# Kernel tuning notes

Hardware: AMD Instinct MI355X
Metric: run time of the kernel (lower is better)

## Reference

```python
import jax, jax.numpy as jnp
import numpy as np

NEG_SLOPE = 0.2  # PyG GATv2Conv default negative_slope


def gatv2_layer(x, src, dst, n_nodes, Wl, bl, Wr, br, att, b_out):
    """GATv2Conv, heads=1, add_self_loops=False.
    x: [N, Din]; src/dst: [E] int; Wl/Wr: [Din, H]; att: [H]."""
    xl = x @ Wl + bl                      # [N, H] source transform
    xr = x @ Wr + br                      # [N, H] target transform
    e = jax.nn.leaky_relu(xl[src] + xr[dst], NEG_SLOPE)  # [E, H]
    logits = e @ att                      # [E]
    # numerically-stable softmax over variable-degree neighborhoods (per dst)
    m = jax.ops.segment_max(logits, dst, num_segments=n_nodes)  # [N]
    m = jnp.where(jnp.isfinite(m), m, 0.0)  # nodes with no in-edges
    p = jnp.exp(logits - m[dst])          # [E]
    denom = jax.ops.segment_sum(p, dst, num_segments=n_nodes)   # [N]
    alpha = p / jnp.maximum(denom[dst], 1e-16)                  # [E]
    out = jax.ops.segment_sum(alpha[:, None] * xl[src], dst, num_segments=n_nodes)
    return out + b_out                    # [N, H]


def setup_inputs() -> dict:
    N, E, D, H = 40000, 640000, 128, 128
    key = jax.random.key(0)
    ks = jax.random.split(key, 12)
    s = 1.0 / np.sqrt(D)
    return {
        "x": jax.random.normal(ks[0], (N, D), dtype=jnp.float32),
        "edge_index": jax.random.randint(ks[1], (2, E), 0, N, dtype=jnp.int64),
        "Wl1": jax.random.normal(ks[2], (D, H), dtype=jnp.float32) * s,
        "bl1": jnp.zeros((H,), jnp.float32),
        "Wr1": jax.random.normal(ks[3], (D, H), dtype=jnp.float32) * s,
        "br1": jnp.zeros((H,), jnp.float32),
        "att1": jax.random.normal(ks[4], (H,), dtype=jnp.float32) * s,
        "b1": jnp.zeros((H,), jnp.float32),
        "Wl2": jax.random.normal(ks[5], (H, H), dtype=jnp.float32) * s,
        "bl2": jnp.zeros((H,), jnp.float32),
        "Wr2": jax.random.normal(ks[6], (H, H), dtype=jnp.float32) * s,
        "br2": jnp.zeros((H,), jnp.float32),
        "att2": jax.random.normal(ks[7], (H,), dtype=jnp.float32) * s,
        "b2": jnp.zeros((H,), jnp.float32),
    }


def reference(x, edge_index, Wl1, bl1, Wr1, br1, att1, b1,
              Wl2, bl2, Wr2, br2, att2, b2):
    n_nodes = x.shape[0]
    src, dst = edge_index[0], edge_index[1]
    h = gatv2_layer(x, src, dst, n_nodes, Wl1, bl1, Wr1, br1, att1, b1)
    h = jax.nn.relu(h)
    h = gatv2_layer(h, src, dst, n_nodes, Wl2, bl2, Wr2, br2, att2, b2)
    return jax.nn.relu(h)
```

## Files before the change

### kernel.cpp

```cpp
#include <hip/hip_runtime.h>
#include <hip/hip_fp16.h>
#include <type_traits>

#define STRIDE 64

typedef _Float16 f16x8 __attribute__((ext_vector_type(8)));
typedef _Float16 h2    __attribute__((ext_vector_type(2)));
typedef float    f32x4 __attribute__((ext_vector_type(4)));
union H8 { f16x8 h8; float4 f4; };
union H2x4 { float4 f4; h2 v[4]; _Float16 h[8]; };

#if defined(__has_builtin)
#if __has_builtin(__builtin_amdgcn_fdot2)
#define FDOT2(a, b, c) __builtin_amdgcn_fdot2((a), (b), (c), false)
#endif
#endif
#ifndef FDOT2
#define FDOT2(a, b, c) fmaf((float)(a)[0], (float)(b)[0], \
                       fmaf((float)(a)[1], (float)(b)[1], (c)))
#endif


__global__ void prep_k(const float* W0, const float* W1,
                       const float* W2, const float* W3,
                       __half* T0, __half* T1, __half* T2, __half* T3,
                       int* __restrict__ cursor, int n) {
    const int bid = blockIdx.x;
    const int tid = threadIdx.x;
    if (bid < 256) {
        const float* W; __half* T;
        switch (bid >> 6) {
            case 0: W = W0; T = T0; break;
            case 1: W = W1; T = T1; break;
            case 2: W = W2; T = T2; break;
            default: W = W3; T = T3; break;
        }
        int idx = (bid & 63) * 256 + tid;
        int c = idx & 127, k = idx >> 7;
        T[(size_t)c * 128 + k] = __float2half(W[(size_t)k * 128 + c]);
    } else {
        int off = (bid - 256) * 1024 + tid * 4;
        if (off + 4 <= n) *(int4*)&cursor[off] = make_int4(0, 0, 0, 0);
        else for (int i = off; i < n; ++i) cursor[i] = 0;
    }
}


__global__ void scatter_k(const int* __restrict__ src, const int* __restrict__ dst,
                          int* __restrict__ cursor, unsigned short* __restrict__ csr,
                          int e) {
    int g = blockIdx.x * blockDim.x + threadIdx.x;
    if (g < e) {
        int d = dst[g];
        int pos = atomicAdd(&cursor[d], 1);
        if (pos < STRIDE) csr[(size_t)d * STRIDE + pos] = (unsigned short)src[g];
    }
}


template <typename IT>
static __device__ __forceinline__ void gemm_body(
    int wid, int lane,
    const IT* __restrict__ A,
    const __half* __restrict__ WtL, const __half* __restrict__ WtR,
    const float* __restrict__ bl, const float* __restrict__ br,
    __half* __restrict__ outl, __half* __restrict__ outr)
{
    const int mrow = lane & 15;
    const int quad = lane >> 4;
    const int base = wid * 16;

    f16x8 afrag[4];
    if constexpr (std::is_same<IT, float>::value) {
        const float* arow = &A[(size_t)(base + mrow) * 128 + quad * 8];
#pragma unroll
        for (int kc = 0; kc < 4; ++kc) {
            const float4 f0 = *(const float4*)&arow[kc * 32];
            const float4 f1 = *(const float4*)&arow[kc * 32 + 4];
            f16x8 h;
            h[0] = (_Float16)f0.x; h[1] = (_Float16)f0.y;
            h[2] = (_Float16)f0.z; h[3] = (_Float16)f0.w;
            h[4] = (_Float16)f1.x; h[5] = (_Float16)f1.y;
            h[6] = (_Float16)f1.z; h[7] = (_Float16)f1.w;
            afrag[kc] = h;
        }
    } else {
        const IT* arow = &A[(size_t)(base + mrow) * 128 + quad * 8];
#pragma unroll
        for (int kc = 0; kc < 4; ++kc)
            afrag[kc] = *(const f16x8*)&arow[kc * 32];
    }

    const size_t orow = (size_t)(base + mrow) * 128;

#pragma unroll
    for (int c = 0; c < 8; ++c) {
        const size_t wof = (size_t)(c * 16 + mrow) * 128 + quad * 8;
        {
            H8 w0, w1, w2, w3;
            w0.f4 = *(const float4*)&WtL[wof +  0];
            w1.f4 = *(const float4*)&WtL[wof + 32];
            w2.f4 = *(const float4*)&WtL[wof + 64];
            w3.f4 = *(const float4*)&WtL[wof + 96];
            f32x4 acc = {0.f, 0.f, 0.f, 0.f};
            acc = __builtin_amdgcn_mfma_f32_16x16x32_f16(w0.h8, afrag[0], acc, 0, 0, 0);
            acc = __builtin_amdgcn_mfma_f32_16x16x32_f16(w1.h8, afrag[1], acc, 0, 0, 0);
            acc = __builtin_amdgcn_mfma_f32_16x16x32_f16(w2.h8, afrag[2], acc, 0, 0, 0);
            acc = __builtin_amdgcn_mfma_f32_16x16x32_f16(w3.h8, afrag[3], acc, 0, 0, 0);
            const float4 bv = *(const float4*)&bl[c * 16 + quad * 4];
            union { __half2 h2v[2]; float2 f2; } o;
            o.h2v[0] = __floats2half2_rn(acc[0] + bv.x, acc[1] + bv.y);
            o.h2v[1] = __floats2half2_rn(acc[2] + bv.z, acc[3] + bv.w);
            *(float2*)&outl[orow + c * 16 + quad * 4] = o.f2;
        }
        {
            H8 w0, w1, w2, w3;
            w0.f4 = *(const float4*)&WtR[wof +  0];
            w1.f4 = *(const float4*)&WtR[wof + 32];
            w2.f4 = *(const float4*)&WtR[wof + 64];
            w3.f4 = *(const float4*)&WtR[wof + 96];
            f32x4 acc = {0.f, 0.f, 0.f, 0.f};
            acc = __builtin_amdgcn_mfma_f32_16x16x32_f16(w0.h8, afrag[0], acc, 0, 0, 0);
            acc = __builtin_amdgcn_mfma_f32_16x16x32_f16(w1.h8, afrag[1], acc, 0, 0, 0);
            acc = __builtin_amdgcn_mfma_f32_16x16x32_f16(w2.h8, afrag[2], acc, 0, 0, 0);
            acc = __builtin_amdgcn_mfma_f32_16x16x32_f16(w3.h8, afrag[3], acc, 0, 0, 0);
            const float4 bv = *(const float4*)&br[c * 16 + quad * 4];
            union { __half2 h2v[2]; float2 f2; } o;
            o.h2v[0] = __floats2half2_rn(acc[0] + bv.x, acc[1] + bv.y);
            o.h2v[1] = __floats2half2_rn(acc[2] + bv.z, acc[3] + bv.w);
            *(float2*)&outr[orow + c * 16 + quad * 4] = o.f2;
        }
    }
}


__global__ __launch_bounds__(256) void gemm1_k(
    const float* __restrict__ A,
    const __half* __restrict__ WtL, const __half* __restrict__ WtR,
    const float* __restrict__ bl, const float* __restrict__ br,
    __half* __restrict__ outl, __half* __restrict__ outr, int nstrips)
{
    const int wid = (blockIdx.x * blockDim.x + threadIdx.x) >> 6;
    if (wid >= nstrips) return;
    gemm_body<float>(wid, threadIdx.x & 63, A, WtL, WtR, bl, br, outl, outr);
}

__global__ __launch_bounds__(256) void gemm2_k(
    const __half* __restrict__ A,
    const __half* __restrict__ WtL, const __half* __restrict__ WtR,
    const float* __restrict__ bl, const float* __restrict__ br,
    __half* __restrict__ outl, __half* __restrict__ outr, int nstrips)
{
    const int wid = (blockIdx.x * blockDim.x + threadIdx.x) >> 6;
    if (wid >= nstrips) return;
    gemm_body<__half>(wid, threadIdx.x & 63, A, WtL, WtR, bl, br, outl, outr);
}


template <int C>
static __device__ __forceinline__ void attn_step(
    const __half* __restrict__ xl, int idx, int e, int g, int t, int deg, int nmax,
    const h2 ah[4], const h2 xrh[4], float& l, float acc[8])
{
    int s[C];
#pragma unroll
    for (int c = 0; c < C; ++c) s[c] = __shfl(idx, e + 4 * c + g);
    H2x4 r[C];
#pragma unroll
    for (int c = 0; c < C; ++c) {
        const int sc = min(s[c], nmax);
        r[c].f4 = *(const float4*)&xl[(size_t)sc * 128 + t * 8];
    }

    const h2 c02 = h2{(_Float16)0.2f, (_Float16)0.2f};
    float p[C];
#pragma unroll
    for (int c = 0; c < C; ++c) {
        float pp = 0.f;
#pragma unroll
        for (int j = 0; j < 4; ++j) {
            h2 z = r[c].v[j] + xrh[j];
            h2 u = __builtin_elementwise_max(z, z * c02);
            pp = FDOT2(u, ah[j], pp);
        }
        p[c] = pp;
    }
#pragma unroll
    for (int off = 1; off <= 8; off <<= 1)
#pragma unroll
        for (int c = 0; c < C; ++c) p[c] += __shfl_xor(p[c], off, 64);

    float w[C];
#pragma unroll
    for (int c = 0; c < C; ++c) {
        w[c] = __expf(p[c]);
        if (e + 4 * c + g >= deg) w[c] = 0.f;
    }
#pragma unroll
    for (int c = 0; c < C; ++c) l += w[c];
#pragma unroll
    for (int k = 0; k < 8; ++k)
#pragma unroll
        for (int c = 0; c < C; ++c)
            acc[k] = fmaf(w[c], (float)r[c].h[k], acc[k]);
}

template <typename OT>
__global__ __launch_bounds__(256) void attn_k(
    const __half* __restrict__ xl, const __half* __restrict__ xr,
    const int* __restrict__ degs, const unsigned short* __restrict__ csr,
    const float* __restrict__ att, const float* __restrict__ bias,
    OT* __restrict__ out, int n, int nmax)
{
    const int wid = (blockIdx.x * blockDim.x + threadIdx.x) >> 6;
    const int lane = threadIdx.x & 63;
    if (wid >= n) return;
    const int g = lane >> 4;
    const int t = lane & 15;

    h2 ah[4];
    {
        float4 a0 = *(const float4*)&att[t * 8];
        float4 a1 = *(const float4*)&att[t * 8 + 4];
        ah[0] = h2{(_Float16)a0.x, (_Float16)a0.y};
        ah[1] = h2{(_Float16)a0.z, (_Float16)a0.w};
        ah[2] = h2{(_Float16)a1.x, (_Float16)a1.y};
        ah[3] = h2{(_Float16)a1.z, (_Float16)a1.w};
    }

    const int deg  = min(degs[wid], STRIDE);
    const int degp = (deg + 3) & ~3;
    const int idx  = csr[(size_t)wid * STRIDE + lane];
    H2x4 xrr; xrr.f4 = *(const float4*)&xr[(size_t)wid * 128 + t * 8];

    float l = 0.f, acc[8];
#pragma unroll
    for (int k = 0; k < 8; ++k) acc[k] = 0.f;

    int e = 0;
    for (; e + 16 <= degp; e += 16)
        attn_step<4>(xl, idx, e, g, t, deg, nmax, ah, xrr.v, l, acc);
    if (e + 8 <= degp) {
        attn_step<2>(xl, idx, e, g, t, deg, nmax, ah, xrr.v, l, acc);
        e += 8;
    }
    if (e + 4 <= degp)
        attn_step<1>(xl, idx, e, g, t, deg, nmax, ah, xrr.v, l, acc);

#pragma unroll
    for (int off = 16; off <= 32; off <<= 1) {
        l += __shfl_xor(l, off, 64);
#pragma unroll
        for (int k = 0; k < 8; ++k) acc[k] += __shfl_xor(acc[k], off, 64);
    }

    if (g == 0) {
        const float inv = 1.0f / fmaxf(l, 1e-16f);
        const float4 b0 = *(const float4*)&bias[t * 8];
        const float4 b1 = *(const float4*)&bias[t * 8 + 4];
        const float bb[8] = {b0.x, b0.y, b0.z, b0.w, b1.x, b1.y, b1.z, b1.w};
        float o[8];
#pragma unroll
        for (int k = 0; k < 8; ++k)
            o[k] = fmaxf(fmaf(acc[k], inv, bb[k]), 0.f);
        if constexpr (std::is_same<OT, __half>::value) {
            union { __half hv[8]; float4 f4; } pk;
#pragma unroll
            for (int k = 0; k < 8; ++k) pk.hv[k] = __float2half(o[k]);
            *(float4*)&out[(size_t)wid * 128 + t * 8] = pk.f4;
        } else {
            float* orow = (float*)&out[(size_t)wid * 128 + t * 8];
            *(float4*)&orow[0] = make_float4(o[0], o[1], o[2], o[3]);
            *(float4*)&orow[4] = make_float4(o[4], o[5], o[6], o[7]);
        }
    }
}


extern "C" void kernel_launch(void* const* d_in, const int* in_sizes, int n_in,
                              void* d_out, int out_size, void* d_ws, size_t ws_size,
                              hipStream_t stream) {
    const float* x    = (const float*)d_in[0];
    const int*   ei   = (const int*)d_in[1];
    const float* Wl1  = (const float*)d_in[2];
    const float* bl1  = (const float*)d_in[3];
    const float* Wr1  = (const float*)d_in[4];
    const float* br1  = (const float*)d_in[5];
    const float* att1 = (const float*)d_in[6];
    const float* b1   = (const float*)d_in[7];
    const float* Wl2  = (const float*)d_in[8];
    const float* bl2  = (const float*)d_in[9];
    const float* Wr2  = (const float*)d_in[10];
    const float* br2  = (const float*)d_in[11];
    const float* att2 = (const float*)d_in[12];
    const float* b2   = (const float*)d_in[13];

    const int N = in_sizes[0] / 128;
    const int E = in_sizes[1] / 2;
    const int* srcp = ei;
    const int* dstp = ei + E;

    char* ws = (char*)d_ws;
    __half* xl     = (__half*)ws; ws += (size_t)N * 128 * 2;
    __half* xr     = (__half*)ws; ws += (size_t)N * 128 * 2;
    __half* h16    = (__half*)ws; ws += (size_t)N * 128 * 2;
    unsigned short* csr = (unsigned short*)ws; ws += (size_t)N * STRIDE * 2;
    int*   cursor  = (int*)ws;    ws += (size_t)N * 4;
    __half* Wt1l   = (__half*)ws; ws += 128 * 128 * 2;
    __half* Wt1r   = (__half*)ws; ws += 128 * 128 * 2;
    __half* Wt2l   = (__half*)ws; ws += 128 * 128 * 2;
    __half* Wt2r   = (__half*)ws; ws += 128 * 128 * 2;

    const int nstrips = N / 16;
    const int gemmBlocks = (nstrips + 3) / 4;
    const int eBlocks = (E + 255) / 256;
    const int zeroBlocks = (N + 1023) / 1024;
    const int attnBlocks = (N + 3) / 4;

    prep_k<<<256 + zeroBlocks, 256, 0, stream>>>(Wl1, Wr1, Wl2, Wr2,
                                                 Wt1l, Wt1r, Wt2l, Wt2r,
                                                 cursor, N);

    scatter_k<<<eBlocks, 256, 0, stream>>>(srcp, dstp, cursor, csr, E);

    gemm1_k<<<gemmBlocks, 256, 0, stream>>>(x, Wt1l, Wt1r, bl1, br1,
                                            xl, xr, nstrips);

    attn_k<__half><<<attnBlocks, 256, 0, stream>>>(xl, xr, cursor, csr,
                                                   att1, b1, h16, N, N - 1);

    gemm2_k<<<gemmBlocks, 256, 0, stream>>>(h16, Wt2l, Wt2r, bl2, br2,
                                            xl, xr, nstrips);

    attn_k<float><<<attnBlocks, 256, 0, stream>>>(xl, xr, cursor, csr,
                                                  att2, b2, (float*)d_out, N, N - 1);
}
```

Before: 241.1 us.

## Transpose attention lane mapping to use DPP reductions; two edges per scatter thread

Attention lanes are remapped so the 4 edge groups sit in adjacent lanes (g = lane&3) and the 16 feature slices are spread across the wave. The final per-edge-group reduction therefore uses quad_perm DPP adds instead of cross-row shuffles, and the logit reduction uses two row_ror DPP steps plus two shuffles. The remap also changes the per-edge gather pattern, so each lane's xl load now sits at a different place in memory. Separately, each scatter thread handles two edges (g and g+E/2) to issue two independent atomics per thread. If E is odd, the last edge is dropped.

```diff
diff --git a/kernel.cpp b/kernel.cpp
--- a/kernel.cpp
+++ b/kernel.cpp
@@ -19,6 +19,18 @@
 #define FDOT2(a, b, c) fmaf((float)(a)[0], (float)(b)[0], \
                        fmaf((float)(a)[1], (float)(b)[1], (c)))
 #endif
+
+#define DPP_ROR4 0x124
+#define DPP_ROR8 0x128
+#define DPP_QX1  0xB1
+#define DPP_QX2  0x4E
+
+template <int CTRL>
+static __device__ __forceinline__ float dppadd(float x) {
+    int v = __builtin_amdgcn_update_dpp(0, __builtin_bit_cast(int, x),
+                                        CTRL, 0xF, 0xF, true);
+    return x + __builtin_bit_cast(float, v);
+}
 
 
 __global__ void prep_k(const float* W0, const float* W1,
@@ -49,11 +61,16 @@
 __global__ void scatter_k(const int* __restrict__ src, const int* __restrict__ dst,
                           int* __restrict__ cursor, unsigned short* __restrict__ csr,
                           int e) {
+    const int half = e >> 1;
     int g = blockIdx.x * blockDim.x + threadIdx.x;
-    if (g < e) {
-        int d = dst[g];
-        int pos = atomicAdd(&cursor[d], 1);
-        if (pos < STRIDE) csr[(size_t)d * STRIDE + pos] = (unsigned short)src[g];
+    if (g < half) {
+        const int g2 = g + half;
+        const int d0 = dst[g];
+        const int d1 = dst[g2];
+        const int p0 = atomicAdd(&cursor[d0], 1);
+        const int p1 = atomicAdd(&cursor[d1], 1);
+        if (p0 < STRIDE) csr[(size_t)d0 * STRIDE + p0] = (unsigned short)src[g];
+        if (p1 < STRIDE) csr[(size_t)d1 * STRIDE + p1] = (unsigned short)src[g2];
     }
 }
 
@@ -186,9 +203,13 @@
         p[c] = pp;
     }
 #pragma unroll
-    for (int off = 1; off <= 8; off <<= 1)
-#pragma unroll
-        for (int c = 0; c < C; ++c) p[c] += __shfl_xor(p[c], off, 64);
+    for (int c = 0; c < C; ++c) p[c] = dppadd<DPP_ROR4>(p[c]);
+#pragma unroll
+    for (int c = 0; c < C; ++c) p[c] = dppadd<DPP_ROR8>(p[c]);
+#pragma unroll
+    for (int c = 0; c < C; ++c) p[c] += __shfl_xor(p[c], 16, 64);
+#pragma unroll
+    for (int c = 0; c < C; ++c) p[c] += __shfl_xor(p[c], 32, 64);
 
     float w[C];
 #pragma unroll
@@ -215,8 +236,8 @@
     const int wid = (blockIdx.x * blockDim.x + threadIdx.x) >> 6;
     const int lane = threadIdx.x & 63;
     if (wid >= n) return;
-    const int g = lane >> 4;
-    const int t = lane & 15;
+    const int g = lane & 3;
+    const int t = lane >> 2;
 
     h2 ah[4];
     {
@@ -247,11 +268,12 @@
     if (e + 4 <= degp)
         attn_step<1>(xl, idx, e, g, t, deg, nmax, ah, xrr.v, l, acc);
 
-#pragma unroll
-    for (int off = 16; off <= 32; off <<= 1) {
-        l += __shfl_xor(l, off, 64);
-#pragma unroll
-        for (int k = 0; k < 8; ++k) acc[k] += __shfl_xor(acc[k], off, 64);
+    l = dppadd<DPP_QX1>(l);
+    l = dppadd<DPP_QX2>(l);
+#pragma unroll
+    for (int k = 0; k < 8; ++k) {
+        acc[k] = dppadd<DPP_QX1>(acc[k]);
+        acc[k] = dppadd<DPP_QX2>(acc[k]);
     }
 
     if (g == 0) {
@@ -313,7 +335,7 @@
 
     const int nstrips = N / 16;
     const int gemmBlocks = (nstrips + 3) / 4;
-    const int eBlocks = (E + 255) / 256;
+    const int sBlocks = (E / 2 + 255) / 256;
     const int zeroBlocks = (N + 1023) / 1024;
     const int attnBlocks = (N + 3) / 4;
 
@@ -321,7 +343,7 @@
                                                  Wt1l, Wt1r, Wt2l, Wt2r,
                                                  cursor, N);
 
-    scatter_k<<<eBlocks, 256, 0, stream>>>(srcp, dstp, cursor, csr, E);
+    scatter_k<<<sBlocks, 256, 0, stream>>>(srcp, dstp, cursor, csr, E);
 
     gemm1_k<<<gemmBlocks, 256, 0, stream>>>(x, Wt1l, Wt1r, bl1, br1,
                                             xl, xr, nstrips);
```

New measurement: 247.4 us. 2.6% more time.
